# Kernel optimization log

Measured on AMD Instinct MI355X. Metric: run time of the kernel, lower is better.

The kernel has to match this reference:

```python
import jax, jax.numpy as jnp
import numpy as np

S, B, D, H, V, MF = 50, 128, 512, 512, 30000, 32
PAD = 0


def setup_inputs() -> dict:
    key = jax.random.key(0)
    ks = jax.random.split(key, 10)
    inp = {
        "user": jax.random.normal(ks[0], (B, MF), dtype=jnp.float32),
        "item": jax.random.normal(ks[1], (B, MF), dtype=jnp.float32),
        "review_input": jax.random.randint(ks[2], (S, B), 0, V, dtype=jnp.int64),
        "review_target": jax.random.randint(ks[3], (S, B), 0, V, dtype=jnp.int64),
        # learned parameters
        "word_emb": jax.random.normal(ks[4], (V, D), dtype=jnp.float32) * 0.02,
        "W_ih": jax.random.normal(ks[5], (3 * H, D), dtype=jnp.float32) * (1.0 / np.sqrt(D)),
        "W_hh": jax.random.normal(ks[6], (3 * H, H), dtype=jnp.float32) * (1.0 / np.sqrt(H)),
        "b_ih": jnp.zeros((3 * H,), dtype=jnp.float32),
        "b_hh": jnp.zeros((3 * H,), dtype=jnp.float32),
        "W_out": jax.random.normal(ks[7], (V, H), dtype=jnp.float32) * (1.0 / np.sqrt(H)),
        "b_out": jnp.zeros((V,), dtype=jnp.float32),
    }
    return inp


def _gru_forward(review_input, word_emb, W_ih, W_hh, b_ih, b_hh, W_out, b_out, batch):
    Hdim = W_hh.shape[1]
    h0 = jnp.zeros((batch, Hdim), dtype=word_emb.dtype)  # encoder returns zeros
    x = word_emb[review_input]  # [S, B, D] embedding lookup (dropout is identity in eval)

    def step(h, x_t):
        gi = x_t @ W_ih.T + b_ih            # [B, 3H]
        gh = h @ W_hh.T + b_hh              # [B, 3H]
        i_r, i_z, i_n = jnp.split(gi, 3, axis=-1)
        h_r, h_z, h_n = jnp.split(gh, 3, axis=-1)
        r = jax.nn.sigmoid(i_r + h_r)
        z = jax.nn.sigmoid(i_z + h_z)
        n = jnp.tanh(i_n + r * h_n)
        h_new = (1.0 - z) * n + z * h
        return h_new, h_new

    _, hs = jax.lax.scan(step, h0, x)       # [S, B, H]
    logits = jnp.einsum('sbh,vh->sbv', hs, W_out) + b_out  # decode from hidden_state
    return logits.reshape(-1, W_out.shape[0])  # [S*B, V], same row order as torch.cat


def reference(user, item, review_input, review_target, word_emb, W_ih, W_hh,
              b_ih, b_hh, W_out, b_out):
    batch = user.shape[0]
    logits = _gru_forward(review_input, word_emb, W_ih, W_hh, b_ih, b_hh,
                          W_out, b_out, batch)
    targets = review_target.reshape(-1)                     # [S*B]
    logp = jax.nn.log_softmax(logits, axis=-1)
    nll = -jnp.take_along_axis(logp, targets[:, None], axis=-1)[:, 0]
    mask = (targets != PAD)
    out_loss = jnp.where(mask, nll, 0.0)                    # reduction='none', ignore_index=PAD
    denom = jnp.maximum(jnp.sum(mask.astype(logits.dtype)), 1.0)
    obj = jnp.sum(out_loss) / denom                         # mean over non-pad tokens
    return (out_loss, obj)
```

## Files before the change

### kernel.cpp

```cpp
#include <hip/hip_runtime.h>
#include <hip/hip_bf16.h>

typedef __attribute__((ext_vector_type(8))) short short8;
typedef __attribute__((ext_vector_type(4))) float floatx4;

#define S_LEN  50
#define BATCH  128
#define DIM    512
#define HID    512
#define G3     1536
#define VOCAB  30000
#define TOKENS 6400
#define NB256  118
#define NVC    472
#define NWG    (25 * NB256)

__device__ __forceinline__ float bf2f(short u) {
    union { unsigned int i; float f; } c;
    c.i = ((unsigned int)(unsigned short)u) << 16;
    return c.f;
}
__device__ __forceinline__ unsigned short f2bf(float x) {
    __hip_bfloat16 h = __float2bfloat16(x);
    unsigned short u;
    __builtin_memcpy(&u, &h, 2);
    return u;
}

__global__ void k_cvt_bf16(const float* __restrict__ src,
                           unsigned short* __restrict__ dst, int n8) {
    int g = blockIdx.x * 256 + threadIdx.x;
    if (g >= n8) return;
    const float* s = src + (size_t)g * 8;
    union { short8 v; unsigned short u[8]; } o;
#pragma unroll
    for (int i = 0; i < 8; ++i) o.u[i] = f2bf(s[i]);
    *(short8*)(dst + (size_t)g * 8) = o.v;
}

__global__ void k_gather_x(const float* __restrict__ emb, const int* __restrict__ idx,
                           unsigned short* __restrict__ X) {
    int g = blockIdx.x * 256 + threadIdx.x;
    int token = g >> 6;
    int chunk = (g & 63) << 3;
    const float* src = emb + (size_t)idx[token] * DIM + chunk;
    union { short8 v; unsigned short u[8]; } o;
#pragma unroll
    for (int i = 0; i < 8; ++i) o.u[i] = f2bf(src[i]);
    *(short8*)(X + (size_t)token * DIM + chunk) = o.v;
}

__launch_bounds__(256)
__global__ void k_gemm_gi(const unsigned short* __restrict__ X,
                          const unsigned short* __restrict__ Wih,
                          const float* __restrict__ b_ih,
                          float* __restrict__ GI) {
    __shared__ unsigned short As[64][72];
    __shared__ unsigned short Bs[64][72];
    int m0 = blockIdx.x * 64;
    int n0 = blockIdx.y * 64;
    int t = threadIdx.x;
    int w = t >> 6, lane = t & 63;
    floatx4 zero = {0.f, 0.f, 0.f, 0.f};
    floatx4 acc[4];
#pragma unroll
    for (int i = 0; i < 4; ++i) acc[i] = zero;
    int srow = t >> 2, scol = (t & 3) * 16;
    for (int k0 = 0; k0 < DIM; k0 += 64) {
        *(short8*)&As[srow][scol]     = *(const short8*)(X   + (size_t)(m0 + srow) * DIM + k0 + scol);
        *(short8*)&As[srow][scol + 8] = *(const short8*)(X   + (size_t)(m0 + srow) * DIM + k0 + scol + 8);
        *(short8*)&Bs[srow][scol]     = *(const short8*)(Wih + (size_t)(n0 + srow) * DIM + k0 + scol);
        *(short8*)&Bs[srow][scol + 8] = *(const short8*)(Wih + (size_t)(n0 + srow) * DIM + k0 + scol + 8);
        __syncthreads();
#pragma unroll
        for (int kt = 0; kt < 2; ++kt) {
            short8 a = *(const short8*)&As[w * 16 + (lane & 15)][kt * 32 + (lane >> 4) * 8];
#pragma unroll
            for (int nt = 0; nt < 4; ++nt) {
                short8 b = *(const short8*)&Bs[nt * 16 + (lane & 15)][kt * 32 + (lane >> 4) * 8];
                acc[nt] = __builtin_amdgcn_mfma_f32_16x16x32_bf16(a, b, acc[nt], 0, 0, 0);
            }
        }
        __syncthreads();
    }
#pragma unroll
    for (int nt = 0; nt < 4; ++nt)
#pragma unroll
        for (int r = 0; r < 4; ++r) {
            int row = m0 + w * 16 + (lane >> 4) * 4 + r;
            int col = n0 + nt * 16 + (lane & 15);
            GI[(size_t)row * G3 + col] = acc[nt][r] + b_ih[col];
        }
}

__launch_bounds__(64)
__global__ void k_gru_step(const float* __restrict__ GI,
                           const unsigned short* __restrict__ Whh,
                           const float* __restrict__ b_hh,
                           float* __restrict__ hf,
                           const unsigned short* __restrict__ hin,
                           unsigned short* __restrict__ hout,
                           int s) {
    int lane = threadIdx.x & 63;
    int bg = blockIdx.x & 7;
    int hs = blockIdx.x >> 3;
    int jc = hs * 16 + (lane & 15);

    const unsigned short* pa  = hin + (size_t)(bg * 16 + (lane & 15)) * HID + (lane >> 4) * 8;
    const unsigned short* pb0 = Whh + (size_t)(0 * HID + jc) * DIM + (lane >> 4) * 8;
    const unsigned short* pb1 = Whh + (size_t)(1 * HID + jc) * DIM + (lane >> 4) * 8;
    const unsigned short* pb2 = Whh + (size_t)(2 * HID + jc) * DIM + (lane >> 4) * 8;

    floatx4 acc0 = {0.f, 0.f, 0.f, 0.f};
    floatx4 acc1 = {0.f, 0.f, 0.f, 0.f};
    floatx4 acc2 = {0.f, 0.f, 0.f, 0.f};
#pragma unroll
    for (int kt = 0; kt < 16; ++kt) {
        short8 a = *(const short8*)(pa + kt * 32);
        acc0 = __builtin_amdgcn_mfma_f32_16x16x32_bf16(a, *(const short8*)(pb0 + kt * 32), acc0, 0, 0, 0);
        acc1 = __builtin_amdgcn_mfma_f32_16x16x32_bf16(a, *(const short8*)(pb1 + kt * 32), acc1, 0, 0, 0);
        acc2 = __builtin_amdgcn_mfma_f32_16x16x32_bf16(a, *(const short8*)(pb2 + kt * 32), acc2, 0, 0, 0);
    }
    float bhr = b_hh[jc], bhz = b_hh[jc + 512], bhn = b_hh[jc + 1024];
#pragma unroll
    for (int r = 0; r < 4; ++r) {
        int brow = bg * 16 + (lane >> 4) * 4 + r;
        int tok = s * BATCH + brow;
        const float* gi = GI + (size_t)tok * G3;
        float rg = 1.f / (1.f + __expf(-(gi[jc] + acc0[r] + bhr)));
        float zg = 1.f / (1.f + __expf(-(gi[jc + 512] + acc1[r] + bhz)));
        float ng = tanhf(gi[jc + 1024] + rg * (acc2[r] + bhn));
        size_t hidx = (size_t)brow * HID + jc;
        float hn = (1.f - zg) * ng + zg * hf[hidx];
        hf[hidx] = hn;
        hout[hidx] = f2bf(hn);
    }
}

__launch_bounds__(1024, 4)
__global__ void k_decode(const unsigned short* __restrict__ HS,
                         const unsigned short* __restrict__ Wout,
                         const float* __restrict__ b_out,
                         float* __restrict__ partial) {
    __shared__ unsigned short As[256 * 64];
    __shared__ unsigned short Bs[256 * 64];

    int bid = blockIdx.x;
    int xcd = bid & 7, pos = bid >> 3;
    int p = (xcd < 6 ? xcd * 369 : 2214 + (xcd - 6) * 368) + pos;
    int sgrp = p / 200;
    int rr   = p - sgrp * 200;
    int mb, nb;
    if (sgrp < 14) { mb = rr >> 3; nb = sgrp * 8 + (rr & 7); }
    else           { int q6 = rr / 6; mb = q6; nb = 112 + (rr - q6 * 6); }
    int m0 = mb * 256, n0 = nb * 256;

    int t = threadIdx.x, w = t >> 6, lane = t & 63;
    int wr = w >> 2, wc = w & 3;

    floatx4 zero = {0.f, 0.f, 0.f, 0.f};
    floatx4 acc[4][4];
#pragma unroll
    for (int mi = 0; mi < 4; ++mi)
#pragma unroll
        for (int ni = 0; ni < 4; ++ni) acc[mi][ni] = zero;

    int srow = t >> 2;
    int scb  = (t & 3) * 32;
    int swz  = (srow & 7) << 4;
    const unsigned short* gA = HS + (size_t)(m0 + srow) * DIM + (t & 3) * 16;
    int vrow = n0 + srow; if (vrow > VOCAB - 1) vrow = VOCAB - 1;
    const unsigned short* gB = Wout + (size_t)vrow * DIM + (t & 3) * 16;
    char* wA0 = (char*)As + ((srow * 128 + scb)      ^ swz);
    char* wA1 = (char*)As + ((srow * 128 + scb + 16) ^ swz);
    char* wB0 = (char*)Bs + ((srow * 128 + scb)      ^ swz);
    char* wB1 = (char*)Bs + ((srow * 128 + scb + 16) ^ swz);

    for (int k0 = 0; k0 < DIM; k0 += 64) {
        short8 a0 = *(const short8*)(gA + k0);
        short8 a1 = *(const short8*)(gA + k0 + 8);
        short8 b0 = *(const short8*)(gB + k0);
        short8 b1 = *(const short8*)(gB + k0 + 8);
        *(short8*)wA0 = a0;
        *(short8*)wA1 = a1;
        *(short8*)wB0 = b0;
        *(short8*)wB1 = b1;
        __syncthreads();
#pragma unroll
        for (int kt = 0; kt < 2; ++kt) {
            short8 af[4], bf[4];
#pragma unroll
            for (int mi = 0; mi < 4; ++mi) {
                int row = wr * 64 + mi * 16 + (lane & 15);
                int off = (row * 128 + kt * 64 + (lane >> 4) * 16) ^ ((row & 7) << 4);
                af[mi] = *(const short8*)((const char*)As + off);
            }
#pragma unroll
            for (int ni = 0; ni < 4; ++ni) {
                int row = wc * 64 + ni * 16 + (lane & 15);
                int off = (row * 128 + kt * 64 + (lane >> 4) * 16) ^ ((row & 7) << 4);
                bf[ni] = *(const short8*)((const char*)Bs + off);
            }
#pragma unroll
            for (int mi = 0; mi < 4; ++mi)
#pragma unroll
                for (int ni = 0; ni < 4; ++ni)
                    acc[mi][ni] = __builtin_amdgcn_mfma_f32_16x16x32_bf16(af[mi], bf[ni], acc[mi][ni], 0, 0, 0);
        }
        __syncthreads();
    }

    float esum[4][4];
#pragma unroll
    for (int mi = 0; mi < 4; ++mi)
#pragma unroll
        for (int r = 0; r < 4; ++r) esum[mi][r] = 0.f;
#pragma unroll
    for (int ni = 0; ni < 4; ++ni) {
        int v = n0 + wc * 64 + ni * 16 + (lane & 15);
        bool ok = v < VOCAB;
        float bo = ok ? b_out[v] : 0.f;
#pragma unroll
        for (int mi = 0; mi < 4; ++mi)
#pragma unroll
            for (int r = 0; r < 4; ++r) {
                float logit = acc[mi][ni][r] + bo;
                esum[mi][r] += ok ? __expf(logit) : 0.f;
            }
    }
#pragma unroll
    for (int d = 1; d < 16; d <<= 1)
#pragma unroll
        for (int mi = 0; mi < 4; ++mi)
#pragma unroll
            for (int r = 0; r < 4; ++r) esum[mi][r] += __shfl_xor(esum[mi][r], d, 64);
    if ((lane & 15) == 0) {
#pragma unroll
        for (int mi = 0; mi < 4; ++mi)
#pragma unroll
            for (int r = 0; r < 4; ++r) {
                int tok = m0 + wr * 64 + mi * 16 + (lane >> 4) * 4 + r;
                partial[(size_t)tok * 512 + nb * 4 + wc] = esum[mi][r];
            }
    }
}

__global__ void k_reduce_lse(const float* __restrict__ partial, float* __restrict__ lse) {
    int tok = blockIdx.x * 4 + (threadIdx.x >> 6);
    int lane = threadIdx.x & 63;
    float s = 0.f;
    for (int j = lane; j < NVC; j += 64) s += partial[(size_t)tok * 512 + j];
#pragma unroll
    for (int d = 1; d < 64; d <<= 1) s += __shfl_xor(s, d, 64);
    if (lane == 0) lse[tok] = logf(s);
}

__global__ void k_tlogit(const unsigned short* __restrict__ HS,
                         const unsigned short* __restrict__ Wout,
                         const float* __restrict__ b_out,
                         const int* __restrict__ target,
                         float* __restrict__ tlg) {
    int tok = blockIdx.x * 4 + (threadIdx.x >> 6);
    int lane = threadIdx.x & 63;
    int tg = target[tok];
    short8 a = *(const short8*)(HS + (size_t)tok * DIM + lane * 8);
    short8 b = *(const short8*)(Wout + (size_t)tg * DIM + lane * 8);
    float s = 0.f;
#pragma unroll
    for (int i = 0; i < 8; ++i) s += bf2f(a[i]) * bf2f(b[i]);
#pragma unroll
    for (int d = 1; d < 64; d <<= 1) s += __shfl_xor(s, d, 64);
    if (lane == 0) tlg[tok] = s + b_out[tg];
}

__global__ void k_finalize(const float* __restrict__ lse, const float* __restrict__ tlg,
                           const int* __restrict__ target, float* __restrict__ out) {
    __shared__ float ssum[256];
    __shared__ float scnt[256];
    int t = threadIdx.x;
    float ls = 0.f, lc = 0.f;
    for (int i = t; i < TOKENS; i += 256) {
        int tg = target[i];
        float loss = (tg != 0) ? (lse[i] - tlg[i]) : 0.f;
        out[i] = loss;
        ls += loss;
        lc += (tg != 0) ? 1.f : 0.f;
    }
    ssum[t] = ls; scnt[t] = lc;
    __syncthreads();
    for (int d = 128; d > 0; d >>= 1) {
        if (t < d) { ssum[t] += ssum[t + d]; scnt[t] += scnt[t + d]; }
        __syncthreads();
    }
    if (t == 0) out[TOKENS] = ssum[0] / fmaxf(scnt[0], 1.f);
}

extern "C" void kernel_launch(void* const* d_in, const int* in_sizes, int n_in,
                              void* d_out, int out_size, void* d_ws, size_t ws_size,
                              hipStream_t stream) {
    const int*   review_input  = (const int*)d_in[2];
    const int*   review_target = (const int*)d_in[3];
    const float* word_emb      = (const float*)d_in[4];
    const float* W_ih          = (const float*)d_in[5];
    const float* W_hh          = (const float*)d_in[6];
    const float* b_ih          = (const float*)d_in[7];
    const float* b_hh          = (const float*)d_in[8];
    const float* W_out         = (const float*)d_in[9];
    const float* b_out         = (const float*)d_in[10];
    float* out = (float*)d_out;

    char* ws = (char*)d_ws;
    size_t off = 0;
    auto alloc = [&](size_t n) { char* p = ws + off; off += (n + 255) & ~(size_t)255; return p; };
    unsigned short* Xb    = (unsigned short*)alloc((size_t)TOKENS * DIM * 2);
    unsigned short* Wihb  = (unsigned short*)alloc((size_t)G3 * DIM * 2);
    unsigned short* Whhb  = (unsigned short*)alloc((size_t)G3 * HID * 2);
    unsigned short* Woutb = (unsigned short*)alloc((size_t)VOCAB * DIM * 2);
    unsigned short* HS    = (unsigned short*)alloc((size_t)TOKENS * HID * 2);
    unsigned short* hzero = (unsigned short*)alloc((size_t)BATCH * HID * 2);
    float* hf      = (float*)alloc((size_t)BATCH * HID * 4);
    float* GI      = (float*)alloc((size_t)TOKENS * G3 * 4);
    float* partial = (float*)alloc((size_t)TOKENS * 512 * 4);
    float* lse     = (float*)alloc((size_t)TOKENS * 4);
    float* tlg     = (float*)alloc((size_t)TOKENS * 4);
    (void)ws_size; (void)in_sizes; (void)n_in; (void)out_size;

    k_cvt_bf16<<<dim3((G3 * DIM / 8 + 255) / 256), dim3(256), 0, stream>>>(W_ih, Wihb, G3 * DIM / 8);
    k_cvt_bf16<<<dim3((G3 * HID / 8 + 255) / 256), dim3(256), 0, stream>>>(W_hh, Whhb, G3 * HID / 8);
    k_cvt_bf16<<<dim3((VOCAB * DIM / 8 + 255) / 256), dim3(256), 0, stream>>>(W_out, Woutb, VOCAB * DIM / 8);
    k_gather_x<<<dim3(TOKENS * DIM / 8 / 256), dim3(256), 0, stream>>>(word_emb, review_input, Xb);

    k_gemm_gi<<<dim3(TOKENS / 64, G3 / 64), dim3(256), 0, stream>>>(Xb, Wihb, b_ih, GI);

    hipMemsetAsync(hf, 0, (size_t)BATCH * HID * 4, stream);
    hipMemsetAsync(hzero, 0, (size_t)BATCH * HID * 2, stream);
    for (int s = 0; s < S_LEN; ++s) {
        const unsigned short* hin = s ? (HS + (size_t)(s - 1) * BATCH * HID) : hzero;
        unsigned short* hout = HS + (size_t)s * BATCH * HID;
        k_gru_step<<<dim3(256), dim3(64), 0, stream>>>(GI, Whhb, b_hh, hf, hin, hout, s);
    }

    k_decode<<<dim3(NWG), dim3(1024), 0, stream>>>(HS, Woutb, b_out, partial);
    k_reduce_lse<<<dim3(TOKENS / 4), dim3(256), 0, stream>>>(partial, lse);
    k_tlogit<<<dim3(TOKENS / 4), dim3(256), 0, stream>>>(HS, Woutb, b_out, review_target, tlg);
    k_finalize<<<dim3(1), dim3(256), 0, stream>>>(lse, tlg, review_target, out);
}
```

Measured before the change: 538.1 us.

## Double-buffer LDS tiles in decode GEMM to overlap global loads with MFMA

Splits the A and B shared-memory tiles of the decode GEMM into two buffers. The next K-slice is loaded from global memory into registers while MFMAs run on the current buffer, then written to the other buffer, leaving one barrier per iteration instead of two. It also precomputes the swizzled LDS read offsets outside the loop. This doubles LDS use to 128 KB per 1024-thread block and adds register pressure from the in-flight loads and offset arrays.

```diff
diff --git a/kernel.cpp b/kernel.cpp
--- a/kernel.cpp
+++ b/kernel.cpp
@@ -142,8 +142,8 @@
                          const unsigned short* __restrict__ Wout,
                          const float* __restrict__ b_out,
                          float* __restrict__ partial) {
-    __shared__ unsigned short As[256 * 64];
-    __shared__ unsigned short Bs[256 * 64];
+    __shared__ unsigned short As[2][256 * 64];
+    __shared__ unsigned short Bs[2][256 * 64];
 
     int bid = blockIdx.x;
     int xcd = bid & 7, pos = bid >> 3;
@@ -171,41 +171,68 @@
     const unsigned short* gA = HS + (size_t)(m0 + srow) * DIM + (t & 3) * 16;
     int vrow = n0 + srow; if (vrow > VOCAB - 1) vrow = VOCAB - 1;
     const unsigned short* gB = Wout + (size_t)vrow * DIM + (t & 3) * 16;
-    char* wA0 = (char*)As + ((srow * 128 + scb)      ^ swz);
-    char* wA1 = (char*)As + ((srow * 128 + scb + 16) ^ swz);
-    char* wB0 = (char*)Bs + ((srow * 128 + scb)      ^ swz);
-    char* wB1 = (char*)Bs + ((srow * 128 + scb + 16) ^ swz);
-
-    for (int k0 = 0; k0 < DIM; k0 += 64) {
-        short8 a0 = *(const short8*)(gA + k0);
-        short8 a1 = *(const short8*)(gA + k0 + 8);
-        short8 b0 = *(const short8*)(gB + k0);
-        short8 b1 = *(const short8*)(gB + k0 + 8);
-        *(short8*)wA0 = a0;
-        *(short8*)wA1 = a1;
-        *(short8*)wB0 = b0;
-        *(short8*)wB1 = b1;
-        __syncthreads();
+    int wo0 = (srow * 128 + scb)      ^ swz;
+    int wo1 = (srow * 128 + scb + 16) ^ swz;
+
+    int roA[4][2], roB[4][2];
+#pragma unroll
+    for (int mi = 0; mi < 4; ++mi)
+#pragma unroll
+        for (int kt = 0; kt < 2; ++kt) {
+            int row = wr * 64 + mi * 16 + (lane & 15);
+            roA[mi][kt] = (row * 128 + kt * 64 + (lane >> 4) * 16) ^ ((row & 7) << 4);
+        }
+#pragma unroll
+    for (int ni = 0; ni < 4; ++ni)
+#pragma unroll
+        for (int kt = 0; kt < 2; ++kt) {
+            int row = wc * 64 + ni * 16 + (lane & 15);
+            roB[ni][kt] = (row * 128 + kt * 64 + (lane >> 4) * 16) ^ ((row & 7) << 4);
+        }
+
+    {
+        short8 a0 = *(const short8*)(gA);
+        short8 a1 = *(const short8*)(gA + 8);
+        short8 b0 = *(const short8*)(gB);
+        short8 b1 = *(const short8*)(gB + 8);
+        *(short8*)((char*)As[0] + wo0) = a0;
+        *(short8*)((char*)As[0] + wo1) = a1;
+        *(short8*)((char*)Bs[0] + wo0) = b0;
+        *(short8*)((char*)Bs[0] + wo1) = b1;
+    }
+    __syncthreads();
+
+    for (int ki = 0; ki < 8; ++ki) {
+        int cur = ki & 1;
+        short8 a0, a1, b0, b1;
+        if (ki < 7) {
+            int k0 = (ki + 1) * 64;
+            a0 = *(const short8*)(gA + k0);
+            a1 = *(const short8*)(gA + k0 + 8);
+            b0 = *(const short8*)(gB + k0);
+            b1 = *(const short8*)(gB + k0 + 8);
+        }
 #pragma unroll
         for (int kt = 0; kt < 2; ++kt) {
             short8 af[4], bf[4];
 #pragma unroll
-            for (int mi = 0; mi < 4; ++mi) {
-                int row = wr * 64 + mi * 16 + (lane & 15);
-                int off = (row * 128 + kt * 64 + (lane >> 4) * 16) ^ ((row & 7) << 4);
-                af[mi] = *(const short8*)((const char*)As + off);
-            }
-#pragma unroll
-            for (int ni = 0; ni < 4; ++ni) {
-                int row = wc * 64 + ni * 16 + (lane & 15);
-                int off = (row * 128 + kt * 64 + (lane >> 4) * 16) ^ ((row & 7) << 4);
-                bf[ni] = *(const short8*)((const char*)Bs + off);
-            }
+            for (int mi = 0; mi < 4; ++mi)
+                af[mi] = *(const short8*)((const char*)As[cur] + roA[mi][kt]);
+#pragma unroll
+            for (int ni = 0; ni < 4; ++ni)
+                bf[ni] = *(const short8*)((const char*)Bs[cur] + roB[ni][kt]);
 #pragma unroll
             for (int mi = 0; mi < 4; ++mi)
 #pragma unroll
                 for (int ni = 0; ni < 4; ++ni)
                     acc[mi][ni] = __builtin_amdgcn_mfma_f32_16x16x32_bf16(af[mi], bf[ni], acc[mi][ni], 0, 0, 0);
+        }
+        if (ki < 7) {
+            int nxt = cur ^ 1;
+            *(short8*)((char*)As[nxt] + wo0) = a0;
+            *(short8*)((char*)As[nxt] + wo1) = a1;
+            *(short8*)((char*)Bs[nxt] + wo0) = b0;
+            *(short8*)((char*)Bs[nxt] + wo1) = b1;
         }
         __syncthreads();
     }
```

Result: no change. 530.9 us (-1.3%).
